# Kernel optimization log

Measured on AMD Instinct MI355X. Metric: run time of the kernel, lower is better.

## Reference

```python
import jax, jax.numpy as jnp
import numpy as np

B, S, D = 2, 2048, 1024   # batch, seq, hidden_size
H = 512                   # intermediate_size
E, K = 8, 2               # num_local_experts, num_experts_per_tok


def setup_inputs() -> dict:
    key = jax.random.key(0)
    k1, k2, k3, k4 = jax.random.split(key, 4)
    scale = 0.02
    return {
        "layer_input": jax.random.normal(k1, (B, S, D), dtype=jnp.float32),
        "w_router": jax.random.normal(k2, (E, D), dtype=jnp.float32) * scale,   # Linear(D, E, bias=False)
        "w_in": jax.random.normal(k3, (E, 2 * H, D), dtype=jnp.float32) * scale,  # ParallelExperts(E, D, 2H)
        "w_out": jax.random.normal(k4, (E, D, H), dtype=jnp.float32) * scale,     # ParallelExperts(E, H, D)
    }


def reference(layer_input, w_router, w_in, w_out):
    bsz, length, d = layer_input.shape
    x = layer_input.reshape(-1, d)                       # [T, D]
    T = x.shape[0]

    # ---- router (JetMoeTopKGating): top-k logits -> softmax gates ----
    router_logits = x @ w_router.T                       # [T, E], fp32
    top_v, top_i = jax.lax.top_k(router_logits, K)       # [T, K]
    top_gates = jax.nn.softmax(top_v, axis=-1)           # [T, K]
    # sparse gate matrix: zero except selected experts (equivalent to
    # torch's sort/gather/index_add dispatch-combine)
    gates = jnp.zeros((T, E), dtype=x.dtype).at[jnp.arange(T)[:, None], top_i].add(top_gates)  # [T, E]

    # ---- experts: fused SwiGLU FFN per expert; combine with sparse gates ----
    h = jnp.einsum('td,efd->tef', x, w_in)               # [T, E, 2H]
    a, b = jnp.split(h, 2, axis=-1)
    h = jax.nn.silu(a) * b                               # [T, E, H]
    y = jnp.einsum('teh,edh->ted', h, w_out)             # [T, E, D]
    out = jnp.einsum('te,ted->td', gates, y)             # [T, D]

    return out.reshape(bsz, length, d), router_logits
```

## Files before the change

### kernel.cpp

```cpp
#include <hip/hip_runtime.h>

typedef unsigned short u16;
typedef unsigned int   u32;

#define T_TOK 4096
#define D_DIM 1024
#define H_DIM 512
#define E_NUM 8
#define NP1   5120
#define MAXP  5120

typedef __bf16 bf16x8 __attribute__((ext_vector_type(8)));
typedef float  f32x4  __attribute__((ext_vector_type(4)));

__device__ __forceinline__ u16 f2bf(float f) {
    return __builtin_bit_cast(u16, (__bf16)f);
}
__device__ __forceinline__ u32 pk2(float a, float b) {
    return (u32)f2bf(a) | ((u32)f2bf(b) << 16);
}
__device__ __forceinline__ float bf2f(u32 lo16) {
    return __builtin_bit_cast(float, lo16 << 16);
}

__device__ __forceinline__ void gll16(const void* g, void* l) {
    __builtin_amdgcn_global_load_lds((const __attribute__((address_space(1))) void*)g,
                                     (__attribute__((address_space(3))) void*)l, 16, 0, 0);
}

#define LDFX(arr, r, ko) __builtin_bit_cast(bf16x8, \
    *(const uint4*)(&arr[r][((((ko) >> 3) ^ ((r) & 7)) << 3)]))
#define MFMA(a, b, c) __builtin_amdgcn_mfma_f32_16x16x32_bf16(a, b, c, 0, 0, 0)

__global__ __launch_bounds__(256) void fused_front(
    const float* __restrict__ x, const float* __restrict__ wr,
    const float* __restrict__ w_in, const float* __restrict__ w_out,
    float* __restrict__ logits_out, int* __restrict__ top_e, float* __restrict__ top_g,
    u16* __restrict__ xb, u16* __restrict__ wib, u16* __restrict__ wob,
    int* __restrict__ e_init, int* __restrict__ blk_hist)
{
    const int bid = blockIdx.x;
    const int tid = threadIdx.x;

    if (bid >= 256) {
        const int b2 = bid - 256;
        if (b2 < 4096) {
            const size_t i = (size_t)b2 * 256 + tid;
            const float4 a = *(const float4*)(w_in + i * 8);
            const float4 b = *(const float4*)(w_in + i * 8 + 4);
            uint4 o;
            o.x = pk2(a.x, a.y); o.y = pk2(a.z, a.w);
            o.z = pk2(b.x, b.y); o.w = pk2(b.z, b.w);
            *(uint4*)(wib + i * 8) = o;
        } else if (b2 < 6144) {
            const size_t i = (size_t)(b2 - 4096) * 256 + tid;
            const float4 a = *(const float4*)(w_out + i * 8);
            const float4 b = *(const float4*)(w_out + i * 8 + 4);
            uint4 o;
            o.x = pk2(a.x, a.y); o.y = pk2(a.z, a.w);
            o.z = pk2(b.x, b.y); o.w = pk2(b.z, b.w);
            *(uint4*)(wob + i * 8) = o;
        } else {
            ((int4*)e_init)[(b2 - 6144) * 256 + tid] = make_int4(-1, -1, -1, -1);
        }
        return;
    }

    __shared__ float wrL[E_NUM][1024];
    __shared__ int   bh[16];
    if (tid < 16) bh[tid] = 0;
    #pragma unroll
    for (int i = 0; i < 8; ++i) {
        const int idx = (i * 256 + tid) * 4;
        *(float4*)&wrL[0][idx] = *(const float4*)(wr + idx);
    }
    __syncthreads();

    const int lane = tid & 63;
    const int wv   = tid >> 6;
    const int t0   = bid * 16 + wv * 4;

    for (int tt = 0; tt < 4; ++tt) {
        const int t = t0 + tt;
        const float* xr = x + ((size_t)t << 10);
        float4 xv[4];
        #pragma unroll
        for (int j = 0; j < 4; ++j)
            xv[j] = *(const float4*)(xr + j * 256 + lane * 4);

        #pragma unroll
        for (int j = 0; j < 4; ++j) {
            uint2 p;
            p.x = pk2(xv[j].x, xv[j].y);
            p.y = pk2(xv[j].z, xv[j].w);
            *(uint2*)(xb + ((size_t)t << 10) + j * 256 + lane * 4) = p;
        }

        float acc[E_NUM];
        #pragma unroll
        for (int e = 0; e < E_NUM; ++e) acc[e] = 0.f;
        #pragma unroll
        for (int j = 0; j < 4; ++j) {
            #pragma unroll
            for (int e = 0; e < E_NUM; ++e) {
                const float4 w4 = *(const float4*)&wrL[e][j * 256 + lane * 4];
                acc[e] += xv[j].x * w4.x + xv[j].y * w4.y + xv[j].z * w4.z + xv[j].w * w4.w;
            }
        }
        #pragma unroll
        for (int off = 32; off >= 1; off >>= 1) {
            #pragma unroll
            for (int e = 0; e < E_NUM; ++e)
                acc[e] += __shfl_xor(acc[e], off);
        }
        if (lane == 0) {
            #pragma unroll
            for (int e = 0; e < E_NUM; ++e)
                logits_out[t * E_NUM + e] = acc[e];
            int i0 = 0; float v0 = acc[0];
            #pragma unroll
            for (int e = 1; e < E_NUM; ++e) { if (acc[e] > v0) { v0 = acc[e]; i0 = e; } }
            int i1 = (i0 == 0) ? 1 : 0; float v1 = acc[i1];
            #pragma unroll
            for (int e = 0; e < E_NUM; ++e) { if (e != i0 && e != i1 && acc[e] > v1) { v1 = acc[e]; i1 = e; } }
            const float ed = __expf(v1 - v0);
            const float g0 = 1.f / (1.f + ed);
            top_e[2 * t]     = i0;  top_e[2 * t + 1] = i1;
            top_g[2 * t]     = g0;  top_g[2 * t + 1] = 1.f - g0;
            atomicAdd(&bh[2 * i0],     1);
            atomicAdd(&bh[2 * i1 + 1], 1);
        }
    }
    __syncthreads();
    if (tid < 16) blk_hist[bid * 16 + tid] = bh[tid];
}

__global__ __launch_bounds__(1024) void prep_kernel(
    const int* __restrict__ top_e, int* __restrict__ ws_i,
    int* __restrict__ e0, int* __restrict__ e1, const int* __restrict__ blk_hist)
{
    __shared__ int hist[16];
    __shared__ int cur[16];
    const int tid = threadIdx.x;
    if (tid < 16) hist[tid] = 0;
    __syncthreads();

    int part = 0;
    #pragma unroll
    for (int j = 0; j < 4; ++j) part += blk_hist[j * 1024 + tid];
    part += __shfl_xor(part, 16);
    part += __shfl_xor(part, 32);
    if ((tid & 63) < 16) atomicAdd(&hist[tid & 15], part);
    __syncthreads();

    if (tid == 0) {
        int off_[16];
        int s0 = 0, s1 = 0;
        for (int e = 0; e < E_NUM; ++e) {
            off_[2 * e]     = s0; s0 += (hist[2 * e]     + 127) & ~127;
            off_[2 * e + 1] = s1; s1 += (hist[2 * e + 1] + 127) & ~127;
        }
        int nt1 = 0;
        for (int e = 0; e < E_NUM; ++e) {
            for (int k = 0; k < 2; ++k) {
                const int b  = 2 * e + k;
                const int pc = (hist[b] + 127) & ~127;
                cur[b] = off_[b];
                for (int j = 0; j < pc / 128; ++j) {
                    const int rl = off_[b] + j * 128;
                    if (nt1 < 96) ws_i[512 + nt1++] = (e << 16) | (k * NP1 + rl);
                }
            }
        }
        ws_i[99] = nt1;
    }
    __syncthreads();

    const int4* t4 = (const int4*)top_e;
    const int4 a = t4[2 * tid];
    const int4 b = t4[2 * tid + 1];
    const int v[8] = {a.x, a.y, a.z, a.w, b.x, b.y, b.z, b.w};
    #pragma unroll
    for (int j = 0; j < 8; ++j) {
        const int i  = tid * 8 + j;
        const int bk = 2 * (v[j] & 7) + (j & 1);
        const int pos = atomicAdd(&cur[bk], 1);
        ((j & 1) ? e1 : e0)[pos] = i;
    }
}

__global__ __launch_bounds__(256, 2) void g1_a(
    const u16* __restrict__ xb, const u16* __restrict__ wib,
    const int* __restrict__ ws_i, const int* __restrict__ e0,
    const int* __restrict__ e1, u16* __restrict__ act)
{
    const int nt  = ws_i[99];
    const int bid = blockIdx.x;
    const int ty  = (bid & 7) * 10 + ((bid >> 3) % 10);
    const int nc  = bid / 80;
    if (ty >= nt) return;
    const int tile = ws_i[512 + ty];
    const int e  = tile >> 16;
    const int rb = tile & 0xFFFF;

    __shared__ __align__(16) u16 xs[128][64];
    __shared__ __align__(16) u16 wt[128][64];
    __shared__ int tokL[128];

    const int tid = threadIdx.x;
    if (tid < 128) {
        const int ent = (rb >= NP1) ? e1[rb - NP1 + tid] : e0[rb + tid];
        tokL[tid] = (ent < 0) ? 0 : (ent >> 1);
    }
    __syncthreads();

    const int wid = tid >> 6, ln = tid & 63, qd = ln >> 4, lm = ln & 15;
    const int wrh = wid >> 1, wch = wid & 1;

    const u16* xsrc[4];
    const u16* wsrc[4];
    const u16* wbase = wib + ((size_t)e << 20);
    #pragma unroll
    for (int j = 0; j < 4; ++j) {
        const int r  = wid * 32 + j * 8 + (ln >> 3);
        const int sg = (ln & 7) ^ (r & 7);
        xsrc[j] = xb + ((size_t)tokL[r] << 10) + (sg << 3);
        const int h = r >> 6, r2 = r & 63;
        const int wrow = (r2 < 32) ? (nc * 64 + h * 32 + r2)
                                   : (512 + nc * 64 + h * 32 + (r2 - 32));
        wsrc[j] = wbase + ((size_t)wrow << 10) + (sg << 3);
    }

    f32x4 acc[4][4];
    #pragma unroll
    for (int i = 0; i < 4; ++i)
        #pragma unroll
        for (int j = 0; j < 4; ++j) acc[i][j] = (f32x4){0.f,0.f,0.f,0.f};

    for (int k0 = 0; k0 < 1024; k0 += 64) {
        #pragma unroll
        for (int j = 0; j < 4; ++j) {
            gll16(xsrc[j] + k0, &xs[wid * 32 + j * 8][0]);
            gll16(wsrc[j] + k0, &wt[wid * 32 + j * 8][0]);
        }
        __syncthreads();
        #pragma unroll
        for (int ki = 0; ki < 2; ++ki) {
            const int ko = ki * 32 + (qd << 3);
            bf16x8 aF[4], bF[4];
            #pragma unroll
            for (int i = 0; i < 4; ++i) aF[i] = LDFX(xs, wrh * 64 + i * 16 + lm, ko);
            #pragma unroll
            for (int j = 0; j < 4; ++j) bF[j] = LDFX(wt, wch * 64 + j * 16 + lm, ko);
            #pragma unroll
            for (int i = 0; i < 4; ++i)
                #pragma unroll
                for (int j = 0; j < 4; ++j)
                    acc[i][j] = MFMA(aF[i], bF[j], acc[i][j]);
        }
        __syncthreads();
    }

    #pragma unroll
    for (int i = 0; i < 4; ++i) {
        #pragma unroll
        for (int j = 0; j < 2; ++j) {
            #pragma unroll
            for (int r = 0; r < 4; ++r) {
                const float a = acc[i][j][r], b = acc[i][j + 2][r];
                const float v = b * a / (1.f + __expf(-a));
                const int row  = wrh * 64 + i * 16 + (qd << 2) + r;
                const int hcol = nc * 64 + wch * 32 + j * 16 + lm;
                act[((size_t)(rb + row) << 9) + hcol] = f2bf(v);
            }
        }
    }
}

__global__ __launch_bounds__(256, 2) void g2_a(
    const u16* __restrict__ act, const u16* __restrict__ wob,
    const int* __restrict__ ws_i, const int* __restrict__ e0,
    const int* __restrict__ e1, const float* __restrict__ top_g,
    u16* __restrict__ y)
{
    const int nt  = ws_i[99];
    const int bid = blockIdx.x;
    const int ty  = (bid & 7) * 10 + ((bid >> 3) % 10);
    const int dc  = bid / 80;
    if (ty >= nt) return;
    const int tile = ws_i[512 + ty];
    const int e  = tile >> 16;
    const int rb = tile & 0xFFFF;

    __shared__ __align__(16) u16 as_[128][64];
    __shared__ __align__(16) u16 wt2[128][64];
    __shared__ int   entL[128];
    __shared__ float gateL[128];

    const int tid = threadIdx.x;
    if (tid < 128) {
        const int ent = (rb >= NP1) ? e1[rb - NP1 + tid] : e0[rb + tid];
        entL[tid]  = ent;
        gateL[tid] = (ent < 0) ? 0.f : top_g[ent];
    }
    __syncthreads();

    const int wid = tid >> 6, ln = tid & 63, qd = ln >> 4, lm = ln & 15;
    const int wrh = wid >> 1, wch = wid & 1;

    const u16* asrc[4];
    const u16* wsrc[4];
    const u16* wbase = wob + ((size_t)e << 19);
    #pragma unroll
    for (int j = 0; j < 4; ++j) {
        const int r  = wid * 32 + j * 8 + (ln >> 3);
        const int sg = (ln & 7) ^ (r & 7);
        asrc[j] = act + ((size_t)(rb + r) << 9) + (sg << 3);
        wsrc[j] = wbase + ((size_t)((dc << 7) + r) << 9) + (sg << 3);
    }

    f32x4 acc[4][4];
    #pragma unroll
    for (int i = 0; i < 4; ++i)
        #pragma unroll
        for (int j = 0; j < 4; ++j) acc[i][j] = (f32x4){0.f,0.f,0.f,0.f};

    for (int k0 = 0; k0 < 512; k0 += 64) {
        #pragma unroll
        for (int j = 0; j < 4; ++j) {
            gll16(asrc[j] + k0, &as_[wid * 32 + j * 8][0]);
            gll16(wsrc[j] + k0, &wt2[wid * 32 + j * 8][0]);
        }
        __syncthreads();
        #pragma unroll
        for (int ki = 0; ki < 2; ++ki) {
            const int ko = ki * 32 + (qd << 3);
            bf16x8 aF[4], bF[4];
            #pragma unroll
            for (int i = 0; i < 4; ++i) aF[i] = LDFX(as_, wrh * 64 + i * 16 + lm, ko);
            #pragma unroll
            for (int j = 0; j < 4; ++j) bF[j] = LDFX(wt2, wch * 64 + j * 16 + lm, ko);
            #pragma unroll
            for (int i = 0; i < 4; ++i)
                #pragma unroll
                for (int j = 0; j < 4; ++j)
                    acc[i][j] = MFMA(aF[i], bF[j], acc[i][j]);
        }
        __syncthreads();
    }

    #pragma unroll
    for (int i = 0; i < 4; ++i) {
        #pragma unroll
        for (int j = 0; j < 4; ++j) {
            #pragma unroll
            for (int r = 0; r < 4; ++r) {
                const int row = wrh * 64 + i * 16 + (qd << 2) + r;
                const int ent = entL[row];
                if (ent >= 0) {
                    const int col = (dc << 7) + wch * 64 + j * 16 + lm;
                    y[((size_t)ent << 10) + col] = f2bf(gateL[row] * acc[i][j][r]);
                }
            }
        }
    }
}

__global__ __launch_bounds__(256) void combine_kernel(
    const u16* __restrict__ y, float* __restrict__ out)
{
    const int idx = blockIdx.x * 256 + threadIdx.x;
    const int t = idx >> 7;
    const int c = (idx & 127) << 3;
    const uint4 a = *(const uint4*)(y + ((size_t)(2 * t)     << 10) + c);
    const uint4 b = *(const uint4*)(y + ((size_t)(2 * t + 1) << 10) + c);
    float4 o0, o1;
    o0.x = bf2f(a.x & 0xFFFFu) + bf2f(b.x & 0xFFFFu);
    o0.y = bf2f(a.x >> 16)     + bf2f(b.x >> 16);
    o0.z = bf2f(a.y & 0xFFFFu) + bf2f(b.y & 0xFFFFu);
    o0.w = bf2f(a.y >> 16)     + bf2f(b.y >> 16);
    o1.x = bf2f(a.z & 0xFFFFu) + bf2f(b.z & 0xFFFFu);
    o1.y = bf2f(a.z >> 16)     + bf2f(b.z >> 16);
    o1.z = bf2f(a.w & 0xFFFFu) + bf2f(b.w & 0xFFFFu);
    o1.w = bf2f(a.w >> 16)     + bf2f(b.w >> 16);
    float* po = out + ((size_t)t << 10) + c;
    *(float4*)po       = o0;
    *(float4*)(po + 4) = o1;
}

extern "C" void kernel_launch(void* const* d_in, const int* in_sizes, int n_in,
                              void* d_out, int out_size, void* d_ws, size_t ws_size,
                              hipStream_t stream)
{
    (void)in_sizes; (void)n_in; (void)out_size; (void)ws_size;
    const float* x     = (const float*)d_in[0];
    const float* wr    = (const float*)d_in[1];
    const float* w_in  = (const float*)d_in[2];
    const float* w_out = (const float*)d_in[3];
    float* out = (float*)d_out;

    char* ws = (char*)d_ws;
    int*   ws_i     = (int*)ws;
    int*   e0       = (int*)(ws + 8192);
    int*   e1       = (int*)(ws + 28672);
    int*   top_e    = (int*)(ws + 49152);
    float* top_g    = (float*)(ws + 81920);
    int*   blk_hist = (int*)(ws + 114688);
    u16*   act      = (u16*)(ws + 147456);
    u16*   xb       = (u16*)(ws + 10633216);
    u16*   wib      = (u16*)(ws + 19021824);
    u16*   y        = (u16*)(ws + 10633216);
    u16*   wob      = (u16*)(ws + 35799040);

    fused_front<<<6410, 256, 0, stream>>>(x, wr, w_in, w_out,
                                          out + (size_t)T_TOK * D_DIM,
                                          top_e, top_g, xb, wib, wob,
                                          e0, blk_hist);
    prep_kernel<<<1, 1024, 0, stream>>>(top_e, ws_i, e0, e1, blk_hist);
    g1_a<<<640, 256, 0, stream>>>(xb, wib, ws_i, e0, e1, act);
    g2_a<<<640, 256, 0, stream>>>(act, wob, ws_i, e0, e1, top_g, y);
    combine_kernel<<<2048, 256, 0, stream>>>(y, out);
}
```

Measured before the change: 166.0 us.

## Double-buffer LDS tiles in expert GEMMs with async global-to-LDS prefetch

```diff
diff --git a/kernel.cpp b/kernel.cpp
--- a/kernel.cpp
+++ b/kernel.cpp
@@ -27,6 +27,14 @@
     __builtin_amdgcn_global_load_lds((const __attribute__((address_space(1))) void*)g,
                                      (__attribute__((address_space(3))) void*)l, 16, 0, 0);
 }
+
+__device__ __forceinline__ void bar() {
+    asm volatile("" ::: "memory");
+    __builtin_amdgcn_s_barrier();
+    asm volatile("" ::: "memory");
+}
+__device__ __forceinline__ void vmw8() { asm volatile("s_waitcnt vmcnt(8)" ::: "memory"); }
+__device__ __forceinline__ void vmw0() { asm volatile("s_waitcnt vmcnt(0)" ::: "memory"); }
 
 #define LDFX(arr, r, ko) __builtin_bit_cast(bf16x8, \
     *(const uint4*)(&arr[r][((((ko) >> 3) ^ ((r) & 7)) << 3)]))
@@ -203,8 +211,8 @@
     const int e  = tile >> 16;
     const int rb = tile & 0xFFFF;
 
-    __shared__ __align__(16) u16 xs[128][64];
-    __shared__ __align__(16) u16 wt[128][64];
+    __shared__ __align__(16) u16 xs[2][128][64];
+    __shared__ __align__(16) u16 wt[2][128][64];
     __shared__ int tokL[128];
 
     const int tid = threadIdx.x;
@@ -237,28 +245,42 @@
         #pragma unroll
         for (int j = 0; j < 4; ++j) acc[i][j] = (f32x4){0.f,0.f,0.f,0.f};
 
-    for (int k0 = 0; k0 < 1024; k0 += 64) {
+    auto STG = [&](int B, int K0) {
         #pragma unroll
         for (int j = 0; j < 4; ++j) {
-            gll16(xsrc[j] + k0, &xs[wid * 32 + j * 8][0]);
-            gll16(wsrc[j] + k0, &wt[wid * 32 + j * 8][0]);
-        }
-        __syncthreads();
+            gll16(xsrc[j] + K0, &xs[B][wid * 32 + j * 8][0]);
+            gll16(wsrc[j] + K0, &wt[B][wid * 32 + j * 8][0]);
+        }
+    };
+    auto CMP = [&](int B) {
         #pragma unroll
         for (int ki = 0; ki < 2; ++ki) {
             const int ko = ki * 32 + (qd << 3);
             bf16x8 aF[4], bF[4];
             #pragma unroll
-            for (int i = 0; i < 4; ++i) aF[i] = LDFX(xs, wrh * 64 + i * 16 + lm, ko);
-            #pragma unroll
-            for (int j = 0; j < 4; ++j) bF[j] = LDFX(wt, wch * 64 + j * 16 + lm, ko);
+            for (int i = 0; i < 4; ++i) aF[i] = LDFX(xs[B], wrh * 64 + i * 16 + lm, ko);
+            #pragma unroll
+            for (int j = 0; j < 4; ++j) bF[j] = LDFX(wt[B], wch * 64 + j * 16 + lm, ko);
             #pragma unroll
             for (int i = 0; i < 4; ++i)
                 #pragma unroll
                 for (int j = 0; j < 4; ++j)
                     acc[i][j] = MFMA(aF[i], bF[j], acc[i][j]);
         }
-        __syncthreads();
+    };
+
+    STG(0, 0);
+    for (int t = 0; t < 16; t += 2) {
+        STG(1, (t + 1) * 64);
+        vmw8();
+        bar();
+        CMP(0);
+        bar();
+        if (t + 2 < 16) { STG(0, (t + 2) * 64); vmw8(); }
+        else            { vmw0(); }
+        bar();
+        CMP(1);
+        bar();
     }
 
     #pragma unroll
@@ -292,8 +314,8 @@
     const int e  = tile >> 16;
     const int rb = tile & 0xFFFF;
 
-    __shared__ __align__(16) u16 as_[128][64];
-    __shared__ __align__(16) u16 wt2[128][64];
+    __shared__ __align__(16) u16 as_[2][128][64];
+    __shared__ __align__(16) u16 wt2[2][128][64];
     __shared__ int   entL[128];
     __shared__ float gateL[128];
 
@@ -325,28 +347,42 @@
         #pragma unroll
         for (int j = 0; j < 4; ++j) acc[i][j] = (f32x4){0.f,0.f,0.f,0.f};
 
-    for (int k0 = 0; k0 < 512; k0 += 64) {
+    auto STG = [&](int B, int K0) {
         #pragma unroll
         for (int j = 0; j < 4; ++j) {
-            gll16(asrc[j] + k0, &as_[wid * 32 + j * 8][0]);
-            gll16(wsrc[j] + k0, &wt2[wid * 32 + j * 8][0]);
-        }
-        __syncthreads();
+            gll16(asrc[j] + K0, &as_[B][wid * 32 + j * 8][0]);
+            gll16(wsrc[j] + K0, &wt2[B][wid * 32 + j * 8][0]);
+        }
+    };
+    auto CMP = [&](int B) {
         #pragma unroll
         for (int ki = 0; ki < 2; ++ki) {
             const int ko = ki * 32 + (qd << 3);
             bf16x8 aF[4], bF[4];
             #pragma unroll
-            for (int i = 0; i < 4; ++i) aF[i] = LDFX(as_, wrh * 64 + i * 16 + lm, ko);
-            #pragma unroll
-            for (int j = 0; j < 4; ++j) bF[j] = LDFX(wt2, wch * 64 + j * 16 + lm, ko);
+            for (int i = 0; i < 4; ++i) aF[i] = LDFX(as_[B], wrh * 64 + i * 16 + lm, ko);
+            #pragma unroll
+            for (int j = 0; j < 4; ++j) bF[j] = LDFX(wt2[B], wch * 64 + j * 16 + lm, ko);
             #pragma unroll
             for (int i = 0; i < 4; ++i)
                 #pragma unroll
                 for (int j = 0; j < 4; ++j)
                     acc[i][j] = MFMA(aF[i], bF[j], acc[i][j]);
         }
-        __syncthreads();
+    };
+
+    STG(0, 0);
+    for (int t = 0; t < 8; t += 2) {
+        STG(1, (t + 1) * 64);
+        vmw8();
+        bar();
+        CMP(0);
+        bar();
+        if (t + 2 < 8) { STG(0, (t + 2) * 64); vmw8(); }
+        else           { vmw0(); }
+        bar();
+        CMP(1);
+        bar();
     }
 
     #pragma unroll
```

Measured after the change: 181.5 us. 9.3% more time.
